# Performance work log

Hardware: AMD Instinct MI355X
Metric: run time of the kernel (lower is better)

Reference implementation:

```python
import jax, jax.numpy as jnp
import numpy as np

IN_F, H, T, NUM_CLASSES, WINDOW_HALF = 14, 24, 25, 4, 12


def _lstm_dir(x_tbf, w_ih, w_hh, b_ih, b_hh, reverse):
    # x_tbf: [T,B,F]; w_ih: [4H,F]; w_hh: [4H,H]; biases: [4H]
    B = x_tbf.shape[1]
    xw = jnp.einsum('tbf,gf->tbg', x_tbf, w_ih) + b_ih + b_hh  # [T,B,4H]

    def step(carry, xw_t):
        h, c = carry
        gates = xw_t + h @ w_hh.T
        i, f, g, o = jnp.split(gates, 4, axis=-1)
        i, f, o = jax.nn.sigmoid(i), jax.nn.sigmoid(f), jax.nn.sigmoid(o)
        g = jnp.tanh(g)
        c = f * c + i * g
        h = o * jnp.tanh(c)
        return (h, c), h

    h0 = jnp.zeros((B, H), x_tbf.dtype)
    c0 = jnp.zeros((B, H), x_tbf.dtype)
    _, hs = jax.lax.scan(step, (h0, c0), xw, reverse=reverse)
    return hs  # [T,B,H], in original time order


def setup_inputs() -> dict:
    key = jax.random.key(0)
    ks = jax.random.split(key, 12)
    s_ih = 1.0 / np.sqrt(H)
    u = lambda k, shape: jax.random.uniform(k, shape, jnp.float32, -s_ih, s_ih)
    return {
        'x': jax.random.normal(ks[0], (65536, T, IN_F), jnp.float32),
        'w_ih_f': u(ks[1], (4 * H, IN_F)),
        'w_hh_f': u(ks[2], (4 * H, H)),
        'b_ih_f': u(ks[3], (4 * H,)),
        'b_hh_f': u(ks[4], (4 * H,)),
        'w_ih_b': u(ks[5], (4 * H, IN_F)),
        'w_hh_b': u(ks[6], (4 * H, H)),
        'b_ih_b': u(ks[7], (4 * H,)),
        'b_hh_b': u(ks[8], (4 * H,)),
        'head_w': u(ks[9], (NUM_CLASSES, 2 * H)),
        'head_b': u(ks[10], (NUM_CLASSES,)),
    }


def reference(x, w_ih_f, w_hh_f, b_ih_f, b_hh_f, w_ih_b, w_hh_b, b_ih_b, b_hh_b, head_w, head_b):
    x_tbf = jnp.transpose(x, (1, 0, 2))  # [T,B,F]
    h_f = _lstm_dir(x_tbf, w_ih_f, w_hh_f, b_ih_f, b_hh_f, reverse=False)
    h_b = _lstm_dir(x_tbf, w_ih_b, w_hh_b, b_ih_b, b_hh_b, reverse=True)
    center = jnp.concatenate([h_f[WINDOW_HALF], h_b[WINDOW_HALF]], axis=-1)  # [B,2H]
    # dropout is identity in eval mode
    return center @ head_w.T + head_b  # [B,4]
```

## Files before the change

kernel.cpp:

```cpp
#include <hip/hip_runtime.h>

typedef __attribute__((ext_vector_type(8))) short frag8;
typedef __attribute__((ext_vector_type(4))) float f4;
typedef __attribute__((ext_vector_type(4))) unsigned int u4;
typedef __attribute__((ext_vector_type(2))) float f2;

namespace {
constexpr int T_STEPS = 25;
constexpr int IN_F    = 14;
constexpr int H       = 24;
constexpr int NSTEP   = 13;
constexpr int CHUNK_B  = 4 * 1024;
constexpr int WAVE_BUF = 2 * CHUNK_B;
constexpr float LOG2E    = 1.4426950408889634f;
constexpr float TWOLOG2E = 2.8853900817779268f;
}

#if __has_builtin(__builtin_amdgcn_exp2f)
#define EXP2F(v) __builtin_amdgcn_exp2f(v)
#else
#define EXP2F(v) __expf(0.6931471805599453f * (v))
#endif

__device__ __forceinline__ unsigned short bf16_rne(float f) {
    unsigned int u = __float_as_uint(f);
    u += 0x7fff + ((u >> 16) & 1);
    return (unsigned short)(u >> 16);
}
__device__ __forceinline__ float bf16_to_f(unsigned short s) {
    return __uint_as_float(((unsigned int)s) << 16);
}
__device__ __forceinline__ float fast_rcp(float x) { return __builtin_amdgcn_rcpf(x); }

__global__ void pack_mfma(const float* __restrict__ wif, const float* __restrict__ whf,
                          const float* __restrict__ bif, const float* __restrict__ bhf,
                          const float* __restrict__ wib, const float* __restrict__ whb,
                          const float* __restrict__ bib, const float* __restrict__ bhb,
                          unsigned short* __restrict__ ws)
{
    const int gid = blockIdx.x * 256 + threadIdx.x;
    if (gid >= 1536) return;
    const int lane = gid & 63;
    const int tile = (gid >> 6) % 6;
    const int set  = (gid / 384) & 1;
    const int dir  = gid / 768;
    const int m = lane & 15, q = lane >> 4;
    const int g = (tile < 4) ? tile : (m & 3);
    const int u_row = (tile < 4) ? m : ((tile == 4 ? 16 : 20) + (m >> 2));
    const float* Wx = dir ? wib : wif;
    const float* Wh = dir ? whb : whf;
    const float* bi = dir ? bib : bif;
    const float* bh = dir ? bhb : bhf;
    const int rowW = g * 24 + u_row;
    const float scale = (g == 2) ? TWOLOG2E : -LOG2E;
    unsigned short vals[8];
    #pragma unroll
    for (int j = 0; j < 8; ++j) {
        const int k = q * 8 + j;
        unsigned short o = 0;
        if (set == 0) {
            if (k < 28) {
                const int f = (k < 14) ? k : k - 14;
                o = bf16_rne(scale * Wx[rowW * IN_F + f]);
            } else if (k < 30) {
                const float b = scale * (bi[rowW] + bh[rowW]);
                const unsigned short hi = bf16_rne(b);
                o = (k == 28) ? hi : bf16_rne(b - bf16_to_f(hi));
            }
        } else {
            const int j7 = k & 7, kq = k >> 3;
            int uh = -1;
            if (j7 < 4)       uh = kq * 4 + j7;
            else if (j7 == 4) uh = 16 + kq;
            else if (j7 == 5) uh = 20 + kq;
            if (uh >= 0) o = bf16_rne(scale * Wh[rowW * H + uh]);
        }
        vals[j] = o;
    }
    unsigned short* d = ws + (size_t)gid * 8;
    #pragma unroll
    for (int j = 0; j < 8; ++j) d[j] = vals[j];
}

__global__ __launch_bounds__(128, 4)
void bilstm_mfma(const float* __restrict__ x, const unsigned short* __restrict__ wpk,
                 const float* __restrict__ head_w, const float* __restrict__ head_b,
                 float* __restrict__ out, int B)
{
    __align__(16) __shared__ unsigned char arena[2 * WAVE_BUF];

    const int tid  = threadIdx.x;
    const int wave = __builtin_amdgcn_readfirstlane(tid >> 6);
    const int lane = tid & 63;
    const int q    = lane >> 4;
    const int col  = lane & 15;
    const int b0   = blockIdx.x * 16;

    frag8 Aw[2][6];
    #pragma unroll
    for (int s = 0; s < 2; ++s)
        #pragma unroll
        for (int t = 0; t < 6; ++t)
            Aw[s][t] = ((const frag8*)wpk)[((wave * 2 + s) * 6 + t) * 64 + lane];

    unsigned char* bufA = arena + wave * WAVE_BUF;
    unsigned char* bufB = bufA + CHUNK_B;

    unsigned int L[IN_F];

    auto stage_load = [&](int c, unsigned int* xu) {
        const int si = c * 4 + (lane >> 4);
        const int e  = lane & 15;
        const int t  = wave ? (T_STEPS - 1 - si) : si;
        const float* xr = x + ((size_t)(b0 + e) * T_STEPS + t) * IN_F;
        #pragma unroll
        for (int i = 0; i < 7; ++i) {
            f2 v = *(const f2*)(xr + 2 * i);
            xu[2*i] = __float_as_uint(v.x); xu[2*i+1] = __float_as_uint(v.y);
        }
    };

    auto stage_write = [&](int c, const unsigned int* xu, unsigned char* buf) {
        if (c == 3 && lane >= 16) return;
        const int sl = lane >> 4;
        const int e  = lane & 15;
        unsigned int lo[IN_F];
        #pragma unroll
        for (int i = 0; i < IN_F; ++i)
            lo[i] = __float_as_uint(__uint_as_float(xu[i])
                                    - __uint_as_float(xu[i] & 0xFFFF0000u));
        unsigned int w[16];
        #pragma unroll
        for (int i = 0; i < 7; ++i)
            w[i] = __builtin_amdgcn_perm(xu[2*i+1], xu[2*i], 0x07060302u);
        w[7] = __builtin_amdgcn_perm(lo[1], lo[0], 0x07060302u);
        #pragma unroll
        for (int i = 0; i < 6; ++i)
            w[8 + i] = __builtin_amdgcn_perm(lo[2*i+3], lo[2*i+2], 0x07060302u);
        w[14] = 0x3F803F80u;
        w[15] = 0u;
        #pragma unroll
        for (int qq = 0; qq < 4; ++qq)
            *(u4*)(buf + sl * 1024 + qq * 256 + e * 16) =
                (u4){w[qq*4], w[qq*4+1], w[qq*4+2], w[qq*4+3]};
    };

    f4    cv = {0.f, 0.f, 0.f, 0.f};
    float c_s[2] = {0.f, 0.f};
    f4    Hv;
    float h_s[2];
    frag8 Bhh, Bhl;
    const f4 zc = {0.f, 0.f, 0.f, 0.f};

    auto gates = [&](const f4* acc) {
        f4 EI, EF, EG, EO, EC;
        #pragma unroll
        for (int r = 0; r < 4; ++r) {
            EI[r] = EXP2F(acc[0][r]);
            EF[r] = EXP2F(acc[1][r]);
            EG[r] = EXP2F(acc[2][r]);
            EO[r] = EXP2F(acc[3][r]);
        }
        const f4 P  = (EI + 1.0f) * (EG + 1.0f);
        const f4 Df = P * (EF + 1.0f);
        f4 Rf;
        #pragma unroll
        for (int r = 0; r < 4; ++r) Rf[r] = fast_rcp(Df[r]);
        cv = (cv * P + (EG - 1.0f) * (EF + 1.0f)) * Rf;
        #pragma unroll
        for (int r = 0; r < 4; ++r) EC[r] = EXP2F(TWOLOG2E * cv[r]);
        const f4 Do = (EO + 1.0f) * (EC + 1.0f);
        f4 Ro;
        #pragma unroll
        for (int r = 0; r < 4; ++r) Ro[r] = fast_rcp(Do[r]);
        Hv = (EC - 1.0f) * Ro;

        #pragma unroll
        for (int s = 0; s < 2; ++s) {
            const float ei = EXP2F(acc[4 + s][0]);
            const float ef = EXP2F(acc[4 + s][1]);
            const float eg = EXP2F(acc[4 + s][2]);
            const float eo = EXP2F(acc[4 + s][3]);
            const float P2 = (1.0f + ei) * (1.0f + eg);
            const float cn = (c_s[s] * P2 + (eg - 1.0f) * (1.0f + ef))
                             * fast_rcp(P2 * (1.0f + ef));
            c_s[s] = cn;
            const float ec = EXP2F(TWOLOG2E * cn);
            h_s[s] = (ec - 1.0f) * fast_rcp((1.0f + eo) * (1.0f + ec));
        }

        f4 Hl;
        #pragma unroll
        for (int r = 0; r < 4; ++r)
            Hl[r] = Hv[r] - __uint_as_float(__float_as_uint(Hv[r]) & 0xFFFF0000u);
        const float hl4 = h_s[0] - __uint_as_float(__float_as_uint(h_s[0]) & 0xFFFF0000u);
        const float hl5 = h_s[1] - __uint_as_float(__float_as_uint(h_s[1]) & 0xFFFF0000u);
        const u4 uh4 = {
            __builtin_amdgcn_perm(__float_as_uint(Hv[1]), __float_as_uint(Hv[0]), 0x07060302u),
            __builtin_amdgcn_perm(__float_as_uint(Hv[3]), __float_as_uint(Hv[2]), 0x07060302u),
            __builtin_amdgcn_perm(__float_as_uint(h_s[1]), __float_as_uint(h_s[0]), 0x07060302u),
            0u};
        const u4 ul4 = {
            __builtin_amdgcn_perm(__float_as_uint(Hl[1]), __float_as_uint(Hl[0]), 0x07060302u),
            __builtin_amdgcn_perm(__float_as_uint(Hl[3]), __float_as_uint(Hl[2]), 0x07060302u),
            __builtin_amdgcn_perm(__float_as_uint(hl5), __float_as_uint(hl4), 0x07060302u),
            0u};
        Bhh = __builtin_bit_cast(frag8, uh4);
        Bhl = __builtin_bit_cast(frag8, ul4);
    };

    auto full_step = [&](const unsigned char* bp, int r) {
        const frag8 Bx = *(const frag8*)(bp + r * 1024 + q * 256 + col * 16);
        f4 acc[6];
        #pragma unroll
        for (int t = 0; t < 6; ++t) {
            acc[t] = __builtin_amdgcn_mfma_f32_16x16x32_bf16(Aw[0][t], Bx,  zc,     0, 0, 0);
            acc[t] = __builtin_amdgcn_mfma_f32_16x16x32_bf16(Aw[1][t], Bhh, acc[t], 0, 0, 0);
            acc[t] = __builtin_amdgcn_mfma_f32_16x16x32_bf16(Aw[1][t], Bhl, acc[t], 0, 0, 0);
        }
        gates(acc);
    };

    stage_load(0, L);
    stage_write(0, L, bufA);
    stage_load(1, L);

    {
        const frag8 Bx = *(const frag8*)(bufA + q * 256 + col * 16);
        f4 acc[6];
        #pragma unroll
        for (int t = 0; t < 6; ++t)
            acc[t] = __builtin_amdgcn_mfma_f32_16x16x32_bf16(Aw[0][t], Bx, zc, 0, 0, 0);
        gates(acc);
    }

    #pragma unroll 1
    for (int r = 1; r < 4; ++r) full_step(bufA, r);

    #pragma unroll 1
    for (int cc = 1; cc <= 2; ++cc) {
        unsigned char* wb = (cc & 1) ? bufB : bufA;
        stage_write(cc, L, wb);
        stage_load(cc + 1, L);
        #pragma unroll 1
        for (int r = 0; r < 4; ++r) full_step(wb, r);
    }

    stage_write(3, L, bufB);
    full_step(bufB, 0);

    unsigned char* hbase = arena + wave * WAVE_BUF;
    *(f4*)(hbase + col * 96 + q * 16) = Hv;
    *(float*)(hbase + col * 96 + 64 + q * 4) = h_s[0];
    *(float*)(hbase + col * 96 + 80 + q * 4) = h_s[1];

    __syncthreads();

    if (tid < 64) {
        const int e = tid >> 2, cls = tid & 3;
        float acc = head_b[cls];
        const float* hf = (const float*)(arena + e * 96);
        const float* hb = (const float*)(arena + WAVE_BUF + e * 96);
        #pragma unroll
        for (int u = 0; u < H; ++u)
            acc += hf[u] * head_w[cls * 2 * H + u] + hb[u] * head_w[cls * 2 * H + H + u];
        out[(size_t)b0 * 4 + tid] = acc;
    }
}

extern "C" void kernel_launch(void* const* d_in, const int* in_sizes, int n_in,
                              void* d_out, int out_size, void* d_ws, size_t ws_size,
                              hipStream_t stream)
{
    const float* x      = (const float*)d_in[0];
    const float* w_ih_f = (const float*)d_in[1];
    const float* w_hh_f = (const float*)d_in[2];
    const float* b_ih_f = (const float*)d_in[3];
    const float* b_hh_f = (const float*)d_in[4];
    const float* w_ih_b = (const float*)d_in[5];
    const float* w_hh_b = (const float*)d_in[6];
    const float* b_ih_b = (const float*)d_in[7];
    const float* b_hh_b = (const float*)d_in[8];
    const float* head_w = (const float*)d_in[9];
    const float* head_b = (const float*)d_in[10];
    float* out = (float*)d_out;
    unsigned short* ws = (unsigned short*)d_ws;

    const int B = in_sizes[0] / (T_STEPS * IN_F);

    hipLaunchKernelGGL(pack_mfma, dim3(6), dim3(256), 0, stream,
                       w_ih_f, w_hh_f, b_ih_f, b_hh_f,
                       w_ih_b, w_hh_b, b_ih_b, b_hh_b, ws);
    hipLaunchKernelGGL(bilstm_mfma, dim3((B + 15) / 16), dim3(128), 0, stream,
                       x, ws, head_w, head_b, out, B);
}
```

Before: 174.6 us.

## Process two interleaved batch groups per wave to hide recurrence latency

Each wave now runs two independent 16-sample LSTM chains at once, interleaving their MFMA chains and gate computations so one chain's dependent latency can overlap the other's work. Blocks cover 32 samples, the grid is halved, the LDS staging buffers are doubled, and launch bounds drop to 2 blocks per SM. This trades occupancy and register pressure for more instruction-level parallelism within each wave.

```diff
diff --git a/kernel.cpp b/kernel.cpp
--- a/kernel.cpp
+++ b/kernel.cpp
@@ -9,9 +9,9 @@
 constexpr int T_STEPS = 25;
 constexpr int IN_F    = 14;
 constexpr int H       = 24;
-constexpr int NSTEP   = 13;
-constexpr int CHUNK_B  = 4 * 1024;
-constexpr int WAVE_BUF = 2 * CHUNK_B;
+constexpr int CHUNK_B   = 4 * 1024;
+constexpr int GROUP_BUF = 2 * CHUNK_B;
+constexpr int WAVE_BUF  = 2 * GROUP_BUF;
 constexpr float LOG2E    = 1.4426950408889634f;
 constexpr float TWOLOG2E = 2.8853900817779268f;
 }
@@ -82,7 +82,71 @@
     for (int j = 0; j < 8; ++j) d[j] = vals[j];
 }
 
-__global__ __launch_bounds__(128, 4)
+__device__ __forceinline__ void lstm_gates(const f4* acc, f4& cv, float& c_s0, float& c_s1,
+                                           f4& Hv, float& h_s0, float& h_s1,
+                                           frag8& Bhh, frag8& Bhl)
+{
+    f4 EI, EF, EG, EO, EC;
+    #pragma unroll
+    for (int r = 0; r < 4; ++r) {
+        EI[r] = EXP2F(acc[0][r]);
+        EF[r] = EXP2F(acc[1][r]);
+        EG[r] = EXP2F(acc[2][r]);
+        EO[r] = EXP2F(acc[3][r]);
+    }
+    const f4 P  = (EI + 1.0f) * (EG + 1.0f);
+    const f4 Df = P * (EF + 1.0f);
+    f4 Rf;
+    #pragma unroll
+    for (int r = 0; r < 4; ++r) Rf[r] = fast_rcp(Df[r]);
+    cv = (cv * P + (EG - 1.0f) * (EF + 1.0f)) * Rf;
+    #pragma unroll
+    for (int r = 0; r < 4; ++r) EC[r] = EXP2F(TWOLOG2E * cv[r]);
+    const f4 Do = (EO + 1.0f) * (EC + 1.0f);
+    f4 Ro;
+    #pragma unroll
+    for (int r = 0; r < 4; ++r) Ro[r] = fast_rcp(Do[r]);
+    Hv = (EC - 1.0f) * Ro;
+
+    float hs[2];
+    float cs[2] = {c_s0, c_s1};
+    #pragma unroll
+    for (int s = 0; s < 2; ++s) {
+        const float ei = EXP2F(acc[4 + s][0]);
+        const float ef = EXP2F(acc[4 + s][1]);
+        const float eg = EXP2F(acc[4 + s][2]);
+        const float eo = EXP2F(acc[4 + s][3]);
+        const float P2 = (1.0f + ei) * (1.0f + eg);
+        const float cn = (cs[s] * P2 + (eg - 1.0f) * (1.0f + ef))
+                         * fast_rcp(P2 * (1.0f + ef));
+        cs[s] = cn;
+        const float ec = EXP2F(TWOLOG2E * cn);
+        hs[s] = (ec - 1.0f) * fast_rcp((1.0f + eo) * (1.0f + ec));
+    }
+    c_s0 = cs[0]; c_s1 = cs[1];
+    h_s0 = hs[0]; h_s1 = hs[1];
+
+    f4 Hl;
+    #pragma unroll
+    for (int r = 0; r < 4; ++r)
+        Hl[r] = Hv[r] - __uint_as_float(__float_as_uint(Hv[r]) & 0xFFFF0000u);
+    const float hl4 = hs[0] - __uint_as_float(__float_as_uint(hs[0]) & 0xFFFF0000u);
+    const float hl5 = hs[1] - __uint_as_float(__float_as_uint(hs[1]) & 0xFFFF0000u);
+    const u4 uh4 = {
+        __builtin_amdgcn_perm(__float_as_uint(Hv[1]), __float_as_uint(Hv[0]), 0x07060302u),
+        __builtin_amdgcn_perm(__float_as_uint(Hv[3]), __float_as_uint(Hv[2]), 0x07060302u),
+        __builtin_amdgcn_perm(__float_as_uint(hs[1]), __float_as_uint(hs[0]), 0x07060302u),
+        0u};
+    const u4 ul4 = {
+        __builtin_amdgcn_perm(__float_as_uint(Hl[1]), __float_as_uint(Hl[0]), 0x07060302u),
+        __builtin_amdgcn_perm(__float_as_uint(Hl[3]), __float_as_uint(Hl[2]), 0x07060302u),
+        __builtin_amdgcn_perm(__float_as_uint(hl5), __float_as_uint(hl4), 0x07060302u),
+        0u};
+    Bhh = __builtin_bit_cast(frag8, uh4);
+    Bhl = __builtin_bit_cast(frag8, ul4);
+}
+
+__global__ __launch_bounds__(128, 2)
 void bilstm_mfma(const float* __restrict__ x, const unsigned short* __restrict__ wpk,
                  const float* __restrict__ head_w, const float* __restrict__ head_b,
                  float* __restrict__ out, int B)
@@ -94,7 +158,7 @@
     const int lane = tid & 63;
     const int q    = lane >> 4;
     const int col  = lane & 15;
-    const int b0   = blockIdx.x * 16;
+    const int b0   = blockIdx.x * 32;
 
     frag8 Aw[2][6];
     #pragma unroll
@@ -103,16 +167,19 @@
         for (int t = 0; t < 6; ++t)
             Aw[s][t] = ((const frag8*)wpk)[((wave * 2 + s) * 6 + t) * 64 + lane];
 
-    unsigned char* bufA = arena + wave * WAVE_BUF;
-    unsigned char* bufB = bufA + CHUNK_B;
-
-    unsigned int L[IN_F];
-
-    auto stage_load = [&](int c, unsigned int* xu) {
+    unsigned char* wbase = arena + wave * WAVE_BUF;
+    unsigned char* bufA0 = wbase;
+    unsigned char* bufB0 = wbase + CHUNK_B;
+    unsigned char* bufA1 = wbase + GROUP_BUF;
+    unsigned char* bufB1 = wbase + GROUP_BUF + CHUNK_B;
+
+    unsigned int L0[IN_F], L1[IN_F];
+
+    auto stage_load = [&](int g, int c, unsigned int* xu) {
         const int si = c * 4 + (lane >> 4);
         const int e  = lane & 15;
         const int t  = wave ? (T_STEPS - 1 - si) : si;
-        const float* xr = x + ((size_t)(b0 + e) * T_STEPS + t) * IN_F;
+        const float* xr = x + ((size_t)(b0 + g * 16 + e) * T_STEPS + t) * IN_F;
         #pragma unroll
         for (int i = 0; i < 7; ++i) {
             f2 v = *(const f2*)(xr + 2 * i);
@@ -145,122 +212,90 @@
                 (u4){w[qq*4], w[qq*4+1], w[qq*4+2], w[qq*4+3]};
     };
 
-    f4    cv = {0.f, 0.f, 0.f, 0.f};
-    float c_s[2] = {0.f, 0.f};
-    f4    Hv;
-    float h_s[2];
-    frag8 Bhh, Bhl;
+    f4    cv0 = {0.f, 0.f, 0.f, 0.f}, cv1 = {0.f, 0.f, 0.f, 0.f};
+    float c0a = 0.f, c0b = 0.f, c1a = 0.f, c1b = 0.f;
+    f4    Hv0, Hv1;
+    float h0a, h0b, h1a, h1b;
+    frag8 Bhh0, Bhl0, Bhh1, Bhl1;
     const f4 zc = {0.f, 0.f, 0.f, 0.f};
 
-    auto gates = [&](const f4* acc) {
-        f4 EI, EF, EG, EO, EC;
-        #pragma unroll
-        for (int r = 0; r < 4; ++r) {
-            EI[r] = EXP2F(acc[0][r]);
-            EF[r] = EXP2F(acc[1][r]);
-            EG[r] = EXP2F(acc[2][r]);
-            EO[r] = EXP2F(acc[3][r]);
+    const int xoff = q * 256 + col * 16;
+
+    auto full_step2 = [&](const unsigned char* bp0, const unsigned char* bp1, int r) {
+        const frag8 Bx0 = *(const frag8*)(bp0 + r * 1024 + xoff);
+        const frag8 Bx1 = *(const frag8*)(bp1 + r * 1024 + xoff);
+        f4 acc0[6], acc1[6];
+        #pragma unroll
+        for (int t = 0; t < 6; ++t) {
+            acc0[t] = __builtin_amdgcn_mfma_f32_16x16x32_bf16(Aw[0][t], Bx0,  zc,      0, 0, 0);
+            acc1[t] = __builtin_amdgcn_mfma_f32_16x16x32_bf16(Aw[0][t], Bx1,  zc,      0, 0, 0);
+            acc0[t] = __builtin_amdgcn_mfma_f32_16x16x32_bf16(Aw[1][t], Bhh0, acc0[t], 0, 0, 0);
+            acc1[t] = __builtin_amdgcn_mfma_f32_16x16x32_bf16(Aw[1][t], Bhh1, acc1[t], 0, 0, 0);
+            acc0[t] = __builtin_amdgcn_mfma_f32_16x16x32_bf16(Aw[1][t], Bhl0, acc0[t], 0, 0, 0);
+            acc1[t] = __builtin_amdgcn_mfma_f32_16x16x32_bf16(Aw[1][t], Bhl1, acc1[t], 0, 0, 0);
         }
-        const f4 P  = (EI + 1.0f) * (EG + 1.0f);
-        const f4 Df = P * (EF + 1.0f);
-        f4 Rf;
-        #pragma unroll
-        for (int r = 0; r < 4; ++r) Rf[r] = fast_rcp(Df[r]);
-        cv = (cv * P + (EG - 1.0f) * (EF + 1.0f)) * Rf;
-        #pragma unroll
-        for (int r = 0; r < 4; ++r) EC[r] = EXP2F(TWOLOG2E * cv[r]);
-        const f4 Do = (EO + 1.0f) * (EC + 1.0f);
-        f4 Ro;
-        #pragma unroll
-        for (int r = 0; r < 4; ++r) Ro[r] = fast_rcp(Do[r]);
-        Hv = (EC - 1.0f) * Ro;
-
-        #pragma unroll
-        for (int s = 0; s < 2; ++s) {
-            const float ei = EXP2F(acc[4 + s][0]);
-            const float ef = EXP2F(acc[4 + s][1]);
-            const float eg = EXP2F(acc[4 + s][2]);
-            const float eo = EXP2F(acc[4 + s][3]);
-            const float P2 = (1.0f + ei) * (1.0f + eg);
-            const float cn = (c_s[s] * P2 + (eg - 1.0f) * (1.0f + ef))
-                             * fast_rcp(P2 * (1.0f + ef));
-            c_s[s] = cn;
-            const float ec = EXP2F(TWOLOG2E * cn);
-            h_s[s] = (ec - 1.0f) * fast_rcp((1.0f + eo) * (1.0f + ec));
+        lstm_gates(acc0, cv0, c0a, c0b, Hv0, h0a, h0b, Bhh0, Bhl0);
+        lstm_gates(acc1, cv1, c1a, c1b, Hv1, h1a, h1b, Bhh1, Bhl1);
+    };
+
+    stage_load(0, 0, L0);
+    stage_load(1, 0, L1);
+    stage_write(0, L0, bufA0);
+    stage_write(0, L1, bufA1);
+    stage_load(0, 1, L0);
+    stage_load(1, 1, L1);
+
+    {
+        const frag8 Bx0 = *(const frag8*)(bufA0 + xoff);
+        const frag8 Bx1 = *(const frag8*)(bufA1 + xoff);
+        f4 acc0[6], acc1[6];
+        #pragma unroll
+        for (int t = 0; t < 6; ++t) {
+            acc0[t] = __builtin_amdgcn_mfma_f32_16x16x32_bf16(Aw[0][t], Bx0, zc, 0, 0, 0);
+            acc1[t] = __builtin_amdgcn_mfma_f32_16x16x32_bf16(Aw[0][t], Bx1, zc, 0, 0, 0);
         }
-
-        f4 Hl;
-        #pragma unroll
-        for (int r = 0; r < 4; ++r)
-            Hl[r] = Hv[r] - __uint_as_float(__float_as_uint(Hv[r]) & 0xFFFF0000u);
-        const float hl4 = h_s[0] - __uint_as_float(__float_as_uint(h_s[0]) & 0xFFFF0000u);
-        const float hl5 = h_s[1] - __uint_as_float(__float_as_uint(h_s[1]) & 0xFFFF0000u);
-        const u4 uh4 = {
-            __builtin_amdgcn_perm(__float_as_uint(Hv[1]), __float_as_uint(Hv[0]), 0x07060302u),
-            __builtin_amdgcn_perm(__float_as_uint(Hv[3]), __float_as_uint(Hv[2]), 0x07060302u),
-            __builtin_amdgcn_perm(__float_as_uint(h_s[1]), __float_as_uint(h_s[0]), 0x07060302u),
-            0u};
-        const u4 ul4 = {
-            __builtin_amdgcn_perm(__float_as_uint(Hl[1]), __float_as_uint(Hl[0]), 0x07060302u),
-            __builtin_amdgcn_perm(__float_as_uint(Hl[3]), __float_as_uint(Hl[2]), 0x07060302u),
-            __builtin_amdgcn_perm(__float_as_uint(hl5), __float_as_uint(hl4), 0x07060302u),
-            0u};
-        Bhh = __builtin_bit_cast(frag8, uh4);
-        Bhl = __builtin_bit_cast(frag8, ul4);
-    };
-
-    auto full_step = [&](const unsigned char* bp, int r) {
-        const frag8 Bx = *(const frag8*)(bp + r * 1024 + q * 256 + col * 16);
-        f4 acc[6];
-        #pragma unroll
-        for (int t = 0; t < 6; ++t) {
-            acc[t] = __builtin_amdgcn_mfma_f32_16x16x32_bf16(Aw[0][t], Bx,  zc,     0, 0, 0);
-            acc[t] = __builtin_amdgcn_mfma_f32_16x16x32_bf16(Aw[1][t], Bhh, acc[t], 0, 0, 0);
-            acc[t] = __builtin_amdgcn_mfma_f32_16x16x32_bf16(Aw[1][t], Bhl, acc[t], 0, 0, 0);
-        }
-        gates(acc);
-    };
-
-    stage_load(0, L);
-    stage_write(0, L, bufA);
-    stage_load(1, L);
-
-    {
-        const frag8 Bx = *(const frag8*)(bufA + q * 256 + col * 16);
-        f4 acc[6];
-        #pragma unroll
-        for (int t = 0; t < 6; ++t)
-            acc[t] = __builtin_amdgcn_mfma_f32_16x16x32_bf16(Aw[0][t], Bx, zc, 0, 0, 0);
-        gates(acc);
+        lstm_gates(acc0, cv0, c0a, c0b, Hv0, h0a, h0b, Bhh0, Bhl0);
+        lstm_gates(acc1, cv1, c1a, c1b, Hv1, h1a, h1b, Bhh1, Bhl1);
     }
 
     #pragma unroll 1
-    for (int r = 1; r < 4; ++r) full_step(bufA, r);
+    for (int r = 1; r < 4; ++r) full_step2(bufA0, bufA1, r);
 
     #pragma unroll 1
     for (int cc = 1; cc <= 2; ++cc) {
-        unsigned char* wb = (cc & 1) ? bufB : bufA;
-        stage_write(cc, L, wb);
-        stage_load(cc + 1, L);
+        unsigned char* wb0 = (cc & 1) ? bufB0 : bufA0;
+        unsigned char* wb1 = (cc & 1) ? bufB1 : bufA1;
+        stage_write(cc, L0, wb0);
+        stage_write(cc, L1, wb1);
+        stage_load(0, cc + 1, L0);
+        stage_load(1, cc + 1, L1);
         #pragma unroll 1
-        for (int r = 0; r < 4; ++r) full_step(wb, r);
-    }
-
-    stage_write(3, L, bufB);
-    full_step(bufB, 0);
-
-    unsigned char* hbase = arena + wave * WAVE_BUF;
-    *(f4*)(hbase + col * 96 + q * 16) = Hv;
-    *(float*)(hbase + col * 96 + 64 + q * 4) = h_s[0];
-    *(float*)(hbase + col * 96 + 80 + q * 4) = h_s[1];
+        for (int r = 0; r < 4; ++r) full_step2(wb0, wb1, r);
+    }
+
+    stage_write(3, L0, bufB0);
+    stage_write(3, L1, bufB1);
+    full_step2(bufB0, bufB1, 0);
+
+    {
+        unsigned char* h0 = wbase + col * 96;
+        *(f4*)(h0 + q * 16) = Hv0;
+        *(float*)(h0 + 64 + q * 4) = h0a;
+        *(float*)(h0 + 80 + q * 4) = h0b;
+        unsigned char* h1 = wbase + 1536 + col * 96;
+        *(f4*)(h1 + q * 16) = Hv1;
+        *(float*)(h1 + 64 + q * 4) = h1a;
+        *(float*)(h1 + 80 + q * 4) = h1b;
+    }
 
     __syncthreads();
 
-    if (tid < 64) {
+    {
         const int e = tid >> 2, cls = tid & 3;
+        const int hoff = (e >> 4) * 1536 + (e & 15) * 96;
         float acc = head_b[cls];
-        const float* hf = (const float*)(arena + e * 96);
-        const float* hb = (const float*)(arena + WAVE_BUF + e * 96);
+        const float* hf = (const float*)(arena + hoff);
+        const float* hb = (const float*)(arena + WAVE_BUF + hoff);
         #pragma unroll
         for (int u = 0; u < H; ++u)
             acc += hf[u] * head_w[cls * 2 * H + u] + hb[u] * head_w[cls * 2 * H + H + u];
@@ -291,6 +326,6 @@
     hipLaunchKernelGGL(pack_mfma, dim3(6), dim3(256), 0, stream,
                        w_ih_f, w_hh_f, b_ih_f, b_hh_f,
                        w_ih_b, w_hh_b, b_ih_b, b_hh_b, ws);
-    hipLaunchKernelGGL(bilstm_mfma, dim3((B + 15) / 16), dim3(128), 0, stream,
+    hipLaunchKernelGGL(bilstm_mfma, dim3((B + 31) / 32), dim3(128), 0, stream,
                        x, ws, head_w, head_b, out, B);
 }
```

Result: slower. 187.7 us (+7.5%).
